# Optimization experiments

Hardware: AMD Instinct MI355X
Metric: run time of the kernel (lower is better)

## Reference

```python
import jax, jax.numpy as jnp
import numpy as np

NUM_VIRUSES = 50000
NUM_DRUGS = 50000
EMBED_DIM = 128
NUM_LAYERS = 3
NUM_INTERACTIONS = 800000  # undirected virus-drug pairs -> 1.6M directed edges


def setup_inputs() -> dict:
    key = jax.random.key(0)
    k1, k2, k3, k4 = jax.random.split(key, 4)
    n_nodes = NUM_VIRUSES + NUM_DRUGS
    # random bipartite interactions (virus -> global drug index)
    v = jax.random.randint(k1, (NUM_INTERACTIONS,), 0, NUM_VIRUSES)
    d = jax.random.randint(k2, (NUM_INTERACTIONS,), 0, NUM_DRUGS) + NUM_VIRUSES
    # symmetric adjacency: both directions
    edge_row = jnp.concatenate([v, d]).astype(jnp.int32)
    edge_col = jnp.concatenate([d, v]).astype(jnp.int32)
    # symmetric normalization D^{-1/2} A D^{-1/2}
    deg = jnp.zeros((n_nodes,), jnp.float32).at[edge_row].add(1.0)
    dinv_sqrt = jnp.where(deg > 0, jax.lax.rsqrt(jnp.maximum(deg, 1.0)), 0.0)
    edge_val = dinv_sqrt[edge_row] * dinv_sqrt[edge_col]
    virus_emb = jax.random.normal(k3, (NUM_VIRUSES, EMBED_DIM), dtype=jnp.float32) * 0.1
    drug_emb = jax.random.normal(k4, (NUM_DRUGS, EMBED_DIM), dtype=jnp.float32) * 0.1
    return {
        "edge_row": edge_row,
        "edge_col": edge_col,
        "edge_val": edge_val,
        "virus_emb": virus_emb,
        "drug_emb": drug_emb,
    }


def reference(edge_row, edge_col, edge_val, virus_emb, drug_emb):
    num_viruses = virus_emb.shape[0]
    n_nodes = num_viruses + drug_emb.shape[0]
    # initial layer-0 embeddings
    x = jnp.concatenate([virus_emb, drug_emb], axis=0)  # [N, D]
    acc = x  # running sum over layers (fused mean)
    h = x
    for _ in range(NUM_LAYERS):
        # SpMM: h <- A_norm @ h  via gather + segment_sum over COO edges
        msgs = edge_val[:, None] * h[edge_col]            # [nnz, D]
        h = jax.ops.segment_sum(msgs, edge_row, num_segments=n_nodes)
        acc = acc + h
    final = acc / jnp.asarray(NUM_LAYERS + 1, acc.dtype)  # mean over L+1 layers
    return final[:num_viruses, :], final[num_viruses:, :]
```

## Files before the change

kernel.cpp:

```cpp
#include <hip/hip_runtime.h>
#include <hip/hip_fp16.h>

static constexpr int D = 128;
static constexpr int RPB_LOG = 10;
static constexpr int RPB = 1 << RPB_LOG;
static constexpr int MAX_BINS = 1024;
static constexpr int CHUNK = 8192;

__global__ void binCount(const int* __restrict__ erow, int* __restrict__ bin_cnt,
                         int E, int nbins) {
    __shared__ int hist[MAX_BINS];
    int t = threadIdx.x;
    int e0 = blockIdx.x * CHUNK;
    for (int i = t; i < nbins; i += 256) hist[i] = 0;
    __syncthreads();
    for (int k = 0; k < CHUNK / 256; ++k) {
        int e = e0 + t + k * 256;
        if (e < E) atomicAdd(&hist[erow[e] >> RPB_LOG], 1);
    }
    __syncthreads();
    for (int b = t; b < nbins; b += 256)
        if (hist[b]) atomicAdd(&bin_cnt[b], hist[b]);
}

__global__ void scanBins(const int* __restrict__ bin_cnt, int* __restrict__ bin_base,
                         int* __restrict__ gcur, int nbins, int E) {
    __shared__ int sm[MAX_BINS];
    int t = threadIdx.x;
    int v = (t < nbins) ? bin_cnt[t] : 0;
    sm[t] = v;
    __syncthreads();
    for (int off = 1; off < MAX_BINS; off <<= 1) {
        int x = sm[t];
        int y = (t >= off) ? sm[t - off] : 0;
        __syncthreads();
        sm[t] = x + y;
        __syncthreads();
    }
    if (t < nbins) {
        int excl = sm[t] - v;
        bin_base[t] = excl;
        gcur[t] = excl;
    }
    if (t == 0) bin_base[nbins] = E;
}

__global__ void binA(const int* __restrict__ erow, const int* __restrict__ ecol,
                     int* __restrict__ gcur, int2* __restrict__ tmp, int E, int nbins) {
    __shared__ int hist[MAX_BINS];
    __shared__ int base[MAX_BINS];
    __shared__ int lcur[MAX_BINS];
    int t = threadIdx.x;
    int e0 = blockIdx.x * CHUNK;
    for (int i = t; i < nbins; i += 256) { hist[i] = 0; lcur[i] = 0; }
    __syncthreads();
    for (int k = 0; k < CHUNK / 256; ++k) {
        int e = e0 + t + k * 256;
        if (e < E) atomicAdd(&hist[erow[e] >> RPB_LOG], 1);
    }
    __syncthreads();
    for (int b = t; b < nbins; b += 256)
        base[b] = hist[b] ? atomicAdd(&gcur[b], hist[b]) : 0;
    __syncthreads();
    for (int k = 0; k < CHUNK / 256; ++k) {
        int e = e0 + t + k * 256;
        if (e < E) {
            int r = erow[e];
            int b = r >> RPB_LOG;
            int pos = base[b] + atomicAdd(&lcur[b], 1);
            tmp[pos] = make_int2(r, ecol[e]);
        }
    }
}

__global__ void binB(const int2* __restrict__ tmp, const int* __restrict__ bin_base,
                     int* __restrict__ row_ptr, float* __restrict__ dinv,
                     float* __restrict__ rdinv, int* __restrict__ col_s,
                     int N, int E, int nbins) {
    __shared__ int cnt[RPB];
    __shared__ int sm[RPB];
    __shared__ int cur[RPB];
    int b = blockIdx.x;
    int r0 = b << RPB_LOG;
    int t = threadIdx.x;
    cnt[t] = 0;
    __syncthreads();
    int start = bin_base[b];
    int end = bin_base[b + 1];
    for (int p = start + t; p < end; p += RPB)
        atomicAdd(&cnt[tmp[p].x - r0], 1);
    __syncthreads();
    int v = cnt[t];
    sm[t] = v;
    __syncthreads();
    for (int off = 1; off < RPB; off <<= 1) {
        int x = sm[t];
        int y = (t >= off) ? sm[t - off] : 0;
        __syncthreads();
        sm[t] = x + y;
        __syncthreads();
    }
    int rp = start + sm[t] - v;
    int r = r0 + t;
    if (r < N) {
        row_ptr[r] = rp;
        dinv[r]  = (v > 0) ? rsqrtf((float)v) : 0.0f;
        rdinv[r] = (v > 0) ? sqrtf((float)v) : 0.0f;
    }
    if (b == 0 && t == 0) row_ptr[N] = E;
    cur[t] = rp;
    __syncthreads();
    for (int p = start + t; p < end; p += RPB) {
        int2 pr = tmp[p];
        int pos = atomicAdd(&cur[pr.x - r0], 1);
        col_s[pos] = pr.y;
    }
}

__global__ void init_g(const float4* __restrict__ vsrc,
                       const float4* __restrict__ dsrc,
                       const float* __restrict__ dinv,
                       __half2* __restrict__ g,
                       long nv4, long total4) {
    long i = (long)blockIdx.x * blockDim.x + threadIdx.x;
    long stride = (long)gridDim.x * blockDim.x;
    for (; i < total4; i += stride) {
        float4 v = (i < nv4) ? vsrc[i] : dsrc[i - nv4];
        float w = dinv[i >> 5];
        g[i * 2]     = __floats2half2_rn(w * v.x, w * v.y);
        g[i * 2 + 1] = __floats2half2_rn(w * v.z, w * v.w);
    }
}

__global__ void spmm_mid(const int* __restrict__ row_ptr, const int* __restrict__ col_s,
                         const float* __restrict__ dinv, const __half2* __restrict__ g,
                         __half2* __restrict__ gnext, int N) {
    int gid = blockIdx.x * blockDim.x + threadIdx.x;
    int r = __builtin_amdgcn_readfirstlane(gid >> 6);
    if (r >= N) return;
    int lane = gid & 63;
    int start = row_ptr[r], end = row_ptr[r + 1];
    float sx = 0.0f, sy = 0.0f;
    int j = start;
    for (; j + 3 < end; j += 4) {
        int c0 = col_s[j], c1 = col_s[j + 1], c2 = col_s[j + 2], c3 = col_s[j + 3];
        float2 v0 = __half22float2(g[(long)c0 * 64 + lane]);
        float2 v1 = __half22float2(g[(long)c1 * 64 + lane]);
        float2 v2 = __half22float2(g[(long)c2 * 64 + lane]);
        float2 v3 = __half22float2(g[(long)c3 * 64 + lane]);
        sx += (v0.x + v1.x) + (v2.x + v3.x);
        sy += (v0.y + v1.y) + (v2.y + v3.y);
    }
    for (; j < end; ++j) {
        float2 v = __half22float2(g[(long)col_s[j] * 64 + lane]);
        sx += v.x;
        sy += v.y;
    }
    float dr = dinv[r];
    float d2 = dr * dr;
    long o = (long)r * 64 + lane;
    gnext[o] = __floats2half2_rn(d2 * sx, d2 * sy);
}

__global__ void spmm_final(const int* __restrict__ row_ptr, const int* __restrict__ col_s,
                           const float* __restrict__ dinv, const float* __restrict__ rdinv,
                           const __half2* __restrict__ g,
                           const __half2* __restrict__ g1,
                           const float2* __restrict__ xv, const float2* __restrict__ xd,
                           int nvRows, float2* __restrict__ out, int N) {
    int gid = blockIdx.x * blockDim.x + threadIdx.x;
    int r = __builtin_amdgcn_readfirstlane(gid >> 6);
    if (r >= N) return;
    int lane = gid & 63;
    int start = row_ptr[r], end = row_ptr[r + 1];
    float sx = 0.0f, sy = 0.0f;
    int j = start;
    for (; j + 3 < end; j += 4) {
        int c0 = col_s[j], c1 = col_s[j + 1], c2 = col_s[j + 2], c3 = col_s[j + 3];
        float2 v0 = __half22float2(g[(long)c0 * 64 + lane]);
        float2 v1 = __half22float2(g[(long)c1 * 64 + lane]);
        float2 v2 = __half22float2(g[(long)c2 * 64 + lane]);
        float2 v3 = __half22float2(g[(long)c3 * 64 + lane]);
        sx += (v0.x + v1.x) + (v2.x + v3.x);
        sy += (v0.y + v1.y) + (v2.y + v3.y);
    }
    for (; j < end; ++j) {
        float2 v = __half22float2(g[(long)col_s[j] * 64 + lane]);
        sx += v.x;
        sy += v.y;
    }
    float dr = dinv[r];
    float h3x = dr * sx, h3y = dr * sy;
    long o = (long)r * 64 + lane;
    float rd = rdinv[r];
    float2 a = (r < nvRows) ? xv[(long)r * 64 + lane]
                            : xd[(long)(r - nvRows) * 64 + lane];
    float2 p1 = __half22float2(g1[o]);
    float2 p2 = __half22float2(g[o]);
    float ox = 0.25f * (a.x + (p1.x + p2.x) * rd + h3x);
    float oy = 0.25f * (a.y + (p1.y + p2.y) * rd + h3y);
    out[o] = make_float2(ox, oy);
}

__global__ void init_copy(const float4* __restrict__ vsrc,
                          const float4* __restrict__ dsrc,
                          float4* __restrict__ h,
                          float4* __restrict__ acc,
                          long nv4, long total4) {
    long i = (long)blockIdx.x * blockDim.x + threadIdx.x;
    long stride = (long)gridDim.x * blockDim.x;
    for (; i < total4; i += stride) {
        float4 v = (i < nv4) ? vsrc[i] : dsrc[i - nv4];
        h[i] = v;
        acc[i] = v;
    }
}

__global__ void spmm_scatter(const int* __restrict__ erow, const int* __restrict__ ecol,
                             const float* __restrict__ eval, const float* __restrict__ h,
                             float* __restrict__ hnext, int E) {
    long tid = (long)blockIdx.x * blockDim.x + threadIdx.x;
    int e = (int)(tid >> 6);
    if (e >= E) return;
    int lane = (int)(tid & 63);
    int r = erow[e], c = ecol[e];
    float w = eval[e];
    const float2* src = reinterpret_cast<const float2*>(h + (long)c * D);
    float2 m = src[lane];
    float* dst = hnext + (long)r * D + lane * 2;
    atomicAdd(dst, w * m.x);
    atomicAdd(dst + 1, w * m.y);
}

__global__ void add_scale(float4* __restrict__ acc, const float4* __restrict__ b,
                          float s, long total4) {
    long i = (long)blockIdx.x * blockDim.x + threadIdx.x;
    long stride = (long)gridDim.x * blockDim.x;
    for (; i < total4; i += stride) {
        float4 a = acc[i];
        float4 v = b[i];
        a.x = (a.x + v.x) * s;
        a.y = (a.y + v.y) * s;
        a.z = (a.z + v.z) * s;
        a.w = (a.w + v.w) * s;
        acc[i] = a;
    }
}

extern "C" void kernel_launch(void* const* d_in, const int* in_sizes, int n_in,
                              void* d_out, int out_size, void* d_ws, size_t ws_size,
                              hipStream_t stream) {
    const int*   erow = (const int*)d_in[0];
    const int*   ecol = (const int*)d_in[1];
    const float* eval = (const float*)d_in[2];
    const float* vemb = (const float*)d_in[3];
    const float* demb = (const float*)d_in[4];

    int  E   = in_sizes[0];
    long nvD = in_sizes[3];
    long ndD = in_sizes[4];
    long ND  = nvD + ndD;
    int  N   = (int)(ND / D);
    int  nvRows = (int)(nvD / D);
    int  nbins = (N + RPB - 1) >> RPB_LOG;

    float* out = (float*)d_out;

    char* w = (char*)d_ws;
    __half* gA = (__half*)w;  w += (size_t)ND * sizeof(__half);
    __half* gB = (__half*)w;  w += (size_t)ND * sizeof(__half);
    __half* gC = (__half*)w;  w += (size_t)ND * sizeof(__half);
    int* col_s    = (int*)w;  w += (size_t)E * sizeof(int);
    int2* tmp     = (int2*)w; w += (size_t)E * sizeof(int2);
    int* row_ptr  = (int*)w;  w += (size_t)(N + 1) * sizeof(int);
    int* bin_cnt  = (int*)w;  w += MAX_BINS * sizeof(int);
    int* bin_base = (int*)w;  w += (MAX_BINS + 1) * sizeof(int);
    int* gcur     = (int*)w;  w += MAX_BINS * sizeof(int);
    float* dinv   = (float*)w; w += (size_t)N * sizeof(float);
    float* rdinv  = (float*)w; w += (size_t)N * sizeof(float);
    size_t needed = (size_t)(w - (char*)d_ws);

    long total4 = ND / 4;
    long nv4    = nvD / 4;
    const int blk = 256;
    const int copyGrid = 2048;

    if (needed <= ws_size && nbins <= MAX_BINS) {
        hipMemsetAsync(bin_cnt, 0, MAX_BINS * sizeof(int), stream);
        int nblkA = (E + CHUNK - 1) / CHUNK;
        hipLaunchKernelGGL(binCount, dim3(nblkA), dim3(256), 0, stream,
                           erow, bin_cnt, E, nbins);
        hipLaunchKernelGGL(scanBins, dim3(1), dim3(1024), 0, stream,
                           bin_cnt, bin_base, gcur, nbins, E);
        hipLaunchKernelGGL(binA, dim3(nblkA), dim3(256), 0, stream,
                           erow, ecol, gcur, tmp, E, nbins);
        hipLaunchKernelGGL(binB, dim3(nbins), dim3(RPB), 0, stream,
                           tmp, bin_base, row_ptr, dinv, rdinv, col_s, N, E, nbins);

        hipLaunchKernelGGL(init_g, dim3(copyGrid), dim3(blk), 0, stream,
                           (const float4*)vemb, (const float4*)demb, dinv,
                           (__half2*)gA, nv4, total4);

        int rgrid = (int)(((long)N * 64 + blk - 1) / blk);
        hipLaunchKernelGGL(spmm_mid, dim3(rgrid), dim3(blk), 0, stream,
                           row_ptr, col_s, dinv, (const __half2*)gA,
                           (__half2*)gB, N);
        hipLaunchKernelGGL(spmm_mid, dim3(rgrid), dim3(blk), 0, stream,
                           row_ptr, col_s, dinv, (const __half2*)gB,
                           (__half2*)gC, N);
        hipLaunchKernelGGL(spmm_final, dim3(rgrid), dim3(blk), 0, stream,
                           row_ptr, col_s, dinv, rdinv,
                           (const __half2*)gC, (const __half2*)gB,
                           (const float2*)vemb, (const float2*)demb,
                           nvRows, (float2*)out, N);
    } else {
        float* bufA = (float*)d_ws;
        float* bufB = bufA + ND;
        hipLaunchKernelGGL(init_copy, dim3(copyGrid), dim3(blk), 0, stream,
                           (const float4*)vemb, (const float4*)demb,
                           (float4*)bufA, (float4*)out, nv4, total4);
        float* cur = bufA;
        float* nxt = bufB;
        for (int l = 0; l < 3; ++l) {
            hipMemsetAsync(nxt, 0, (size_t)ND * sizeof(float), stream);
            long threads = (long)E * 64;
            int  sgrid   = (int)((threads + blk - 1) / blk);
            hipLaunchKernelGGL(spmm_scatter, dim3(sgrid), dim3(blk), 0, stream,
                               erow, ecol, eval, cur, nxt, E);
            float s = (l == 2) ? 0.25f : 1.0f;
            hipLaunchKernelGGL(add_scale, dim3(copyGrid), dim3(blk), 0, stream,
                               (float4*)out, (const float4*)nxt, s, total4);
            float* t = cur; cur = nxt; nxt = t;
        }
    }
}
```

Baseline: 266.0 us.

## Split each wavefront into four edge groups with 16-byte vector gathers

The SpMM gather kernels now split each 64-lane wavefront into four 16-lane groups. Each group processes a different neighbor edge and loads a full 256-byte fp16 row with 16-byte vector loads. Partial sums are combined with cross-lane shuffles, and only 16 lanes write the result. This gives more independent row fetches in flight per wave and wider memory transactions. In exchange it adds shuffle reductions and leaves lanes idle in the epilogue and on rows with few edges.

```diff
diff --git a/kernel.cpp b/kernel.cpp
--- a/kernel.cpp
+++ b/kernel.cpp
@@ -132,74 +132,105 @@
     }
 }
 
+__device__ __forceinline__ void gather_rows(const int* __restrict__ col_s,
+                                            int start, int end,
+                                            const __half* __restrict__ gsrc,
+                                            int grp, int sub, float acc[8]) {
+    int j = start + grp;
+    for (; j + 4 < end; j += 8) {
+        int c0 = col_s[j];
+        int c1 = col_s[j + 4];
+        float4 v0 = ((const float4*)(gsrc + (long)c0 * D))[sub];
+        float4 v1 = ((const float4*)(gsrc + (long)c1 * D))[sub];
+        const __half2* h0 = (const __half2*)&v0;
+        const __half2* h1 = (const __half2*)&v1;
+#pragma unroll
+        for (int k = 0; k < 4; ++k) {
+            float2 f0 = __half22float2(h0[k]);
+            float2 f1 = __half22float2(h1[k]);
+            acc[2 * k]     += f0.x + f1.x;
+            acc[2 * k + 1] += f0.y + f1.y;
+        }
+    }
+    if (j < end) {
+        int c = col_s[j];
+        float4 v = ((const float4*)(gsrc + (long)c * D))[sub];
+        const __half2* h = (const __half2*)&v;
+#pragma unroll
+        for (int k = 0; k < 4; ++k) {
+            float2 f = __half22float2(h[k]);
+            acc[2 * k]     += f.x;
+            acc[2 * k + 1] += f.y;
+        }
+    }
+#pragma unroll
+    for (int k = 0; k < 8; ++k) {
+        acc[k] += __shfl_xor(acc[k], 16, 64);
+        acc[k] += __shfl_xor(acc[k], 32, 64);
+    }
+}
+
 __global__ void spmm_mid(const int* __restrict__ row_ptr, const int* __restrict__ col_s,
-                         const float* __restrict__ dinv, const __half2* __restrict__ g,
-                         __half2* __restrict__ gnext, int N) {
+                         const float* __restrict__ dinv, const __half* __restrict__ g,
+                         __half* __restrict__ gnext, int N) {
     int gid = blockIdx.x * blockDim.x + threadIdx.x;
     int r = __builtin_amdgcn_readfirstlane(gid >> 6);
     if (r >= N) return;
     int lane = gid & 63;
+    int grp = lane >> 4, sub = lane & 15;
     int start = row_ptr[r], end = row_ptr[r + 1];
-    float sx = 0.0f, sy = 0.0f;
-    int j = start;
-    for (; j + 3 < end; j += 4) {
-        int c0 = col_s[j], c1 = col_s[j + 1], c2 = col_s[j + 2], c3 = col_s[j + 3];
-        float2 v0 = __half22float2(g[(long)c0 * 64 + lane]);
-        float2 v1 = __half22float2(g[(long)c1 * 64 + lane]);
-        float2 v2 = __half22float2(g[(long)c2 * 64 + lane]);
-        float2 v3 = __half22float2(g[(long)c3 * 64 + lane]);
-        sx += (v0.x + v1.x) + (v2.x + v3.x);
-        sy += (v0.y + v1.y) + (v2.y + v3.y);
-    }
-    for (; j < end; ++j) {
-        float2 v = __half22float2(g[(long)col_s[j] * 64 + lane]);
-        sx += v.x;
-        sy += v.y;
-    }
-    float dr = dinv[r];
-    float d2 = dr * dr;
-    long o = (long)r * 64 + lane;
-    gnext[o] = __floats2half2_rn(d2 * sx, d2 * sy);
+    float acc[8] = {0, 0, 0, 0, 0, 0, 0, 0};
+    gather_rows(col_s, start, end, g, grp, sub, acc);
+    if (lane < 16) {
+        float dr = dinv[r];
+        float d2 = dr * dr;
+        float4 st;
+        __half2* hs = (__half2*)&st;
+#pragma unroll
+        for (int k = 0; k < 4; ++k)
+            hs[k] = __floats2half2_rn(d2 * acc[2 * k], d2 * acc[2 * k + 1]);
+        ((float4*)(gnext + (long)r * D))[sub] = st;
+    }
 }
 
 __global__ void spmm_final(const int* __restrict__ row_ptr, const int* __restrict__ col_s,
                            const float* __restrict__ dinv, const float* __restrict__ rdinv,
-                           const __half2* __restrict__ g,
-                           const __half2* __restrict__ g1,
-                           const float2* __restrict__ xv, const float2* __restrict__ xd,
-                           int nvRows, float2* __restrict__ out, int N) {
+                           const __half* __restrict__ g2,
+                           const __half* __restrict__ g1,
+                           const float* __restrict__ xv, const float* __restrict__ xd,
+                           int nvRows, float* __restrict__ out, int N) {
     int gid = blockIdx.x * blockDim.x + threadIdx.x;
     int r = __builtin_amdgcn_readfirstlane(gid >> 6);
     if (r >= N) return;
     int lane = gid & 63;
+    int grp = lane >> 4, sub = lane & 15;
     int start = row_ptr[r], end = row_ptr[r + 1];
-    float sx = 0.0f, sy = 0.0f;
-    int j = start;
-    for (; j + 3 < end; j += 4) {
-        int c0 = col_s[j], c1 = col_s[j + 1], c2 = col_s[j + 2], c3 = col_s[j + 3];
-        float2 v0 = __half22float2(g[(long)c0 * 64 + lane]);
-        float2 v1 = __half22float2(g[(long)c1 * 64 + lane]);
-        float2 v2 = __half22float2(g[(long)c2 * 64 + lane]);
-        float2 v3 = __half22float2(g[(long)c3 * 64 + lane]);
-        sx += (v0.x + v1.x) + (v2.x + v3.x);
-        sy += (v0.y + v1.y) + (v2.y + v3.y);
-    }
-    for (; j < end; ++j) {
-        float2 v = __half22float2(g[(long)col_s[j] * 64 + lane]);
-        sx += v.x;
-        sy += v.y;
-    }
-    float dr = dinv[r];
-    float h3x = dr * sx, h3y = dr * sy;
-    long o = (long)r * 64 + lane;
-    float rd = rdinv[r];
-    float2 a = (r < nvRows) ? xv[(long)r * 64 + lane]
-                            : xd[(long)(r - nvRows) * 64 + lane];
-    float2 p1 = __half22float2(g1[o]);
-    float2 p2 = __half22float2(g[o]);
-    float ox = 0.25f * (a.x + (p1.x + p2.x) * rd + h3x);
-    float oy = 0.25f * (a.y + (p1.y + p2.y) * rd + h3y);
-    out[o] = make_float2(ox, oy);
+    float acc[8] = {0, 0, 0, 0, 0, 0, 0, 0};
+    gather_rows(col_s, start, end, g2, grp, sub, acc);
+    if (lane < 16) {
+        float dr = dinv[r];
+        float rd = rdinv[r];
+        const float* xbase = (r < nvRows) ? (xv + (long)r * D)
+                                          : (xd + (long)(r - nvRows) * D);
+        float4 x0 = ((const float4*)xbase)[sub * 2];
+        float4 x1 = ((const float4*)xbase)[sub * 2 + 1];
+        float4 p1v = ((const float4*)(g1 + (long)r * D))[sub];
+        float4 p2v = ((const float4*)(g2 + (long)r * D))[sub];
+        const __half2* h1 = (const __half2*)&p1v;
+        const __half2* h2 = (const __half2*)&p2v;
+        float xr[8] = {x0.x, x0.y, x0.z, x0.w, x1.x, x1.y, x1.z, x1.w};
+        float o[8];
+#pragma unroll
+        for (int k = 0; k < 4; ++k) {
+            float2 f1 = __half22float2(h1[k]);
+            float2 f2 = __half22float2(h2[k]);
+            o[2 * k]     = 0.25f * (xr[2 * k]     + (f1.x + f2.x) * rd + dr * acc[2 * k]);
+            o[2 * k + 1] = 0.25f * (xr[2 * k + 1] + (f1.y + f2.y) * rd + dr * acc[2 * k + 1]);
+        }
+        float4* ob = (float4*)(out + (long)r * D);
+        ob[sub * 2]     = make_float4(o[0], o[1], o[2], o[3]);
+        ob[sub * 2 + 1] = make_float4(o[4], o[5], o[6], o[7]);
+    }
 }
 
 __global__ void init_copy(const float4* __restrict__ vsrc,
@@ -303,16 +334,12 @@
 
         int rgrid = (int)(((long)N * 64 + blk - 1) / blk);
         hipLaunchKernelGGL(spmm_mid, dim3(rgrid), dim3(blk), 0, stream,
-                           row_ptr, col_s, dinv, (const __half2*)gA,
-                           (__half2*)gB, N);
+                           row_ptr, col_s, dinv, gA, gB, N);
         hipLaunchKernelGGL(spmm_mid, dim3(rgrid), dim3(blk), 0, stream,
-                           row_ptr, col_s, dinv, (const __half2*)gB,
-                           (__half2*)gC, N);
+                           row_ptr, col_s, dinv, gB, gC, N);
         hipLaunchKernelGGL(spmm_final, dim3(rgrid), dim3(blk), 0, stream,
-                           row_ptr, col_s, dinv, rdinv,
-                           (const __half2*)gC, (const __half2*)gB,
-                           (const float2*)vemb, (const float2*)demb,
-                           nvRows, (float2*)out, N);
+                           row_ptr, col_s, dinv, rdinv, gC, gB,
+                           vemb, demb, nvRows, out, N);
     } else {
         float* bufA = (float*)d_ws;
         float* bufB = bufA + ND;
```

Result: no change. 266.0 us (+0.0%).
